# Kernel optimization log

Measured on AMD Instinct MI355X. Metric: run time of the kernel, lower is better.

## Reference

```python
import jax, jax.numpy as jnp
import numpy as np

B, S, D, H, DFF = 2, 4096, 256, 8, 1024
DK = D // H


def setup_inputs() -> dict:
    key = jax.random.key(0)
    ks = jax.random.split(key, 12)
    sc = 0.02
    inp = {
        "x": jax.random.normal(ks[0], (B, S, D), jnp.float32),
        "mask": jnp.ones((B, 1, 1, S), jnp.int32),
        "Wq": jax.random.normal(ks[1], (D, D), jnp.float32) * sc,
        "bq": jnp.zeros((D,), jnp.float32),
        "Wk": jax.random.normal(ks[2], (D, D), jnp.float32) * sc,
        "bk": jnp.zeros((D,), jnp.float32),
        "Wv": jax.random.normal(ks[3], (D, D), jnp.float32) * sc,
        "bv": jnp.zeros((D,), jnp.float32),
        "Wo": jax.random.normal(ks[4], (D, D), jnp.float32) * sc,
        "bo": jnp.zeros((D,), jnp.float32),
        "W1": jax.random.normal(ks[5], (D, DFF), jnp.float32) * sc,
        "b1": jnp.zeros((DFF,), jnp.float32),
        "W2": jax.random.normal(ks[6], (DFF, D), jnp.float32) * sc,
        "b2": jnp.zeros((D,), jnp.float32),
        "g1": jnp.ones((D,), jnp.float32),
        "be1": jnp.zeros((D,), jnp.float32),
        "g2": jnp.ones((D,), jnp.float32),
        "be2": jnp.zeros((D,), jnp.float32),
        "a1": jnp.float32(1e-8),
        "a2": jnp.float32(1e-8),
    }
    return inp


def _layernorm(x, g, b, eps=1e-5):
    mu = jnp.mean(x, axis=-1, keepdims=True)
    var = jnp.var(x, axis=-1, keepdims=True)
    return (x - mu) * jax.lax.rsqrt(var + eps) * g + b


def _block(x, mask, Wq, bq, Wk, bk, Wv, bv, Wo, bo, W1, b1, W2, b2, g1, be1, g2, be2, a1, a2):
    # multi-head attention (dropout = identity in eval)
    def proj(W, b):
        return (x @ W + b).reshape(B, S, H, DK).transpose(0, 2, 1, 3)  # [B,H,S,DK]
    q, k, v = proj(Wq, bq), proj(Wk, bk), proj(Wv, bv)
    scores = jnp.einsum("bhsd,bhtd->bhst", q, k) / jnp.sqrt(jnp.float32(DK))
    scores = jnp.where(mask == 0, jnp.float32(-1e9), scores)
    p_attn = jax.nn.softmax(scores, axis=-1)
    ctx = jnp.einsum("bhst,bhtd->bhsd", p_attn, v)
    ctx = ctx.transpose(0, 2, 1, 3).reshape(B, S, D)
    attn_out = ctx @ Wo + bo
    x1 = _layernorm(x + a1 * attn_out, g1, be1)
    # FFN
    h = jax.nn.gelu(x1 @ W1 + b1, approximate=False)
    ffn_out = h @ W2 + b2
    return _layernorm(x1 + a2 * ffn_out, g2, be2)


def reference(x, mask, Wq, bq, Wk, bk, Wv, bv, Wo, bo, W1, b1, W2, b2, g1, be1, g2, be2, a1, a2):
    return _block(x, mask, Wq, bq, Wk, bk, Wv, bv, Wo, bo, W1, b1, W2, b2, g1, be1, g2, be2, a1, a2)
```

## Files before the change

### kernel.cpp

```cpp
#include <hip/hip_runtime.h>
#include <hip/hip_bf16.h>
#include <math.h>

#define B_ 2
#define S_ 4096
#define D_ 256
#define H_ 8
#define DFF_ 1024
#define DK_ 32

typedef __attribute__((ext_vector_type(8))) short short8;
typedef __attribute__((ext_vector_type(4))) float f32x4;
typedef __attribute__((ext_vector_type(16))) float f32x16;
typedef __attribute__((ext_vector_type(4))) int int4v;

__device__ __forceinline__ unsigned short f2bf(float f) {
  unsigned int u = __builtin_bit_cast(unsigned int, f);
  u += 0x7FFFu + ((u >> 16) & 1u);
  return (unsigned short)(u >> 16);
}

__device__ __forceinline__ float bf2f(unsigned short s) {
  unsigned int u = ((unsigned int)s) << 16;
  return __builtin_bit_cast(float, u);
}

__device__ __forceinline__ short8 u32x4_to_s8(unsigned int a, unsigned int b,
                                              unsigned int c, unsigned int d) {
  int4v v = {(int)a, (int)b, (int)c, (int)d};
  return __builtin_bit_cast(short8, v);
}

__device__ __forceinline__ float gelu_fast(float v) {
  float e = __builtin_amdgcn_exp2f(v * fmaf(0.10294609f, v * v, 2.3022077f));
  float th = 1.0f - 2.0f * __builtin_amdgcn_rcpf(e + 1.0f);
  return 0.5f * v * (1.0f + th);
}

__global__ __launch_bounds__(256) void k_prepw(
    const float* __restrict__ Wq, const float* __restrict__ Wk,
    const float* __restrict__ Wv, const float* __restrict__ Wo,
    const float* __restrict__ W1, const float* __restrict__ W2,
    const float* __restrict__ bq, const float* __restrict__ bk,
    const float* __restrict__ bv, const float* __restrict__ x,
    unsigned short* __restrict__ WqkvT, unsigned short* __restrict__ WoT,
    unsigned short* __restrict__ W1T, unsigned short* __restrict__ W2T,
    float* __restrict__ bqkv, unsigned short* __restrict__ xb) {
  const float k2 = 0.25500525551f;
  int bx = blockIdx.x, t = threadIdx.x;

  if (bx < 192) {
    __shared__ float tile[64][65];
    const float* src;
    unsigned short* dst;
    int Ksz, Nsz, ti, tj;
    float scale = 1.0f;
    if (bx < 48) {
      int which = bx >> 4, s = bx & 15;
      src = (which == 0) ? Wq : (which == 1) ? Wk : Wv;
      dst = WqkvT + which * 65536;
      Ksz = 256; Nsz = 256; ti = s >> 2; tj = s & 3;
      if (which == 0) scale = k2;
    } else if (bx < 64) {
      int s = bx - 48;
      src = Wo; dst = WoT; Ksz = 256; Nsz = 256; ti = s >> 2; tj = s & 3;
    } else if (bx < 128) {
      int s = bx - 64;
      src = W1; dst = W1T; Ksz = 256; Nsz = 1024; ti = s >> 4; tj = s & 15;
    } else {
      int s = bx - 128;
      src = W2; dst = W2T; Ksz = 1024; Nsz = 256; ti = s >> 2; tj = s & 3;
    }
    int row0 = ti * 64, col0 = tj * 64;
    int c = t & 63, rg = t >> 6;
#pragma unroll
    for (int i = 0; i < 16; i++) {
      int rr = rg * 16 + i;
      tile[rr][c] = src[(size_t)(row0 + rr) * Nsz + col0 + c] * scale;
    }
    __syncthreads();
    int k = t & 63;
#pragma unroll
    for (int i = 0; i < 16; i++) {
      int nn = rg * 16 + i;
      dst[(size_t)(col0 + nn) * Ksz + row0 + k] = f2bf(tile[k][nn]);
    }
  } else if (bx == 192) {
#pragma unroll
    for (int j = 0; j < 3; j++) {
      int i = j * 256 + t;
      if (i < 768)
        bqkv[i] = (i < 256) ? bq[i] * k2 : (i < 512) ? bk[i - 256] : bv[i - 512];
    }
  } else {
    int i = (bx - 193) * 2048 + t * 8;
    f32x4 f0 = *(const f32x4*)(x + i);
    f32x4 f1 = *(const f32x4*)(x + i + 4);
    short8 o;
#pragma unroll
    for (int e = 0; e < 4; e++) { o[e] = (short)f2bf(f0[e]); o[e + 4] = (short)f2bf(f1[e]); }
    *(short8*)(xb + i) = o;
  }
}

__global__ __launch_bounds__(256) void k_gemmqkv(const unsigned short* __restrict__ A,
                                                 const unsigned short* __restrict__ Bt,
                                                 const float* __restrict__ bias,
                                                 unsigned short* __restrict__ qb,
                                                 unsigned short* __restrict__ kpk,
                                                 unsigned short* __restrict__ vpk) {
  const int K = 256;
  __shared__ unsigned short Al[128][40];
  __shared__ unsigned short Bl[128][40];
  const int tid = threadIdx.x;
  const int wid = tid >> 6, lane = tid & 63;
  const int lhi = lane >> 4, llo = lane & 15;
  const int wr = wid >> 1, wc = wid & 1;
  const int rowbase = wr * 64, colbase = wc * 64;
  const int bm = blockIdx.x, bn = blockIdx.y;

  f32x4 zero = {0.f, 0.f, 0.f, 0.f};
  f32x4 acc[4][4];
#pragma unroll
  for (int m = 0; m < 4; m++)
#pragma unroll
    for (int n = 0; n < 4; n++) acc[m][n] = zero;

  const int r0 = tid >> 2, c8 = (tid & 3) * 8;
  const unsigned short* A16a = A + (size_t)(bm * 128 + r0) * K + c8;
  const unsigned short* A16b = A + (size_t)(bm * 128 + r0 + 64) * K + c8;
  const unsigned short* Brow0 = Bt + (size_t)(bn * 128 + r0) * K + c8;
  const unsigned short* Brow1 = Bt + (size_t)(bn * 128 + r0 + 64) * K + c8;

  for (int kb = 0; kb < K; kb += 32) {
    __syncthreads();
    *(short8*)&Al[r0][c8] = *(const short8*)(A16a + kb);
    *(short8*)&Al[r0 + 64][c8] = *(const short8*)(A16b + kb);
    *(short8*)&Bl[r0][c8] = *(const short8*)(Brow0 + kb);
    *(short8*)&Bl[r0 + 64][c8] = *(const short8*)(Brow1 + kb);
    __syncthreads();
    short8 af[4], bf[4];
#pragma unroll
    for (int m = 0; m < 4; m++) af[m] = *(const short8*)&Al[rowbase + m * 16 + llo][lhi * 8];
#pragma unroll
    for (int n = 0; n < 4; n++) bf[n] = *(const short8*)&Bl[colbase + n * 16 + llo][lhi * 8];
#pragma unroll
    for (int m = 0; m < 4; m++)
#pragma unroll
      for (int n = 0; n < 4; n++)
        acc[m][n] = __builtin_amdgcn_mfma_f32_16x16x32_bf16(af[m], bf[n], acc[m][n], 0, 0, 0);
  }

#pragma unroll
  for (int m = 0; m < 4; m++)
#pragma unroll
    for (int n = 0; n < 4; n++)
#pragma unroll
      for (int r = 0; r < 4; r++) {
        int row = bm * 128 + rowbase + m * 16 + lhi * 4 + r;
        int gcol = bn * 128 + colbase + n * 16 + llo;
        int which = gcol >> 8;
        int col0 = gcol & 255;
        float v = acc[m][n][r] + bias[gcol];
        unsigned short bv = f2bf(v);
        int t = row & (S_ - 1), b = row >> 12;
        int h = col0 >> 5;
        if (which == 0) {
          qb[(size_t)row * 256 + col0] = bv;
        } else if (which == 1) {
          int c5 = col0 & 31, jj = (c5 >> 4) & 1, hik = (c5 >> 3) & 1, e = c5 & 7;
          int tile = t >> 6, i = (t >> 5) & 1, l31k = t & 31;
          size_t addr = (((size_t)(b * 8 + h) * 64 + tile) * 4 + i * 2 + jj) * 512 +
                        (hik * 32 + l31k) * 8 + e;
          kpk[addr] = bv;
        } else {
          int d = col0 & 31;
          int x5 = t >> 6, j = (t >> 3) & 7, kk = t & 7;
          size_t addr = (((size_t)(b * 8 + h) * 64 + x5) * 4 + (j >> 1)) * 512 +
                        ((j & 1) * 32 + d) * 8 + kk;
          vpk[addr] = bv;
        }
      }
}

__global__ __launch_bounds__(256) void k_gemm1(const unsigned short* __restrict__ A,
                                               const unsigned short* __restrict__ Bt,
                                               const float* __restrict__ bias,
                                               unsigned short* __restrict__ Cout,
                                               int M, int N, int K) {
  __shared__ unsigned short Al[128][40];
  __shared__ unsigned short Bl[128][40];
  const int tid = threadIdx.x;
  const int wid = tid >> 6, lane = tid & 63;
  const int lhi = lane >> 4, llo = lane & 15;
  const int wr = wid >> 1, wc = wid & 1;
  const int rowbase = wr * 64, colbase = wc * 64;
  const int bm = blockIdx.x, bn = blockIdx.y;

  f32x4 zero = {0.f, 0.f, 0.f, 0.f};
  f32x4 acc[4][4];
#pragma unroll
  for (int m = 0; m < 4; m++)
#pragma unroll
    for (int n = 0; n < 4; n++) acc[m][n] = zero;

  const int r0 = tid >> 2, c8 = (tid & 3) * 8;
  const unsigned short* A16a = A + (size_t)(bm * 128 + r0) * K + c8;
  const unsigned short* A16b = A + (size_t)(bm * 128 + r0 + 64) * K + c8;
  const unsigned short* Brow0 = Bt + (size_t)(bn * 128 + r0) * K + c8;
  const unsigned short* Brow1 = Bt + (size_t)(bn * 128 + r0 + 64) * K + c8;

  for (int kb = 0; kb < K; kb += 32) {
    __syncthreads();
    *(short8*)&Al[r0][c8] = *(const short8*)(A16a + kb);
    *(short8*)&Al[r0 + 64][c8] = *(const short8*)(A16b + kb);
    *(short8*)&Bl[r0][c8] = *(const short8*)(Brow0 + kb);
    *(short8*)&Bl[r0 + 64][c8] = *(const short8*)(Brow1 + kb);
    __syncthreads();
    short8 af[4], bf[4];
#pragma unroll
    for (int m = 0; m < 4; m++) af[m] = *(const short8*)&Al[rowbase + m * 16 + llo][lhi * 8];
#pragma unroll
    for (int n = 0; n < 4; n++) bf[n] = *(const short8*)&Bl[colbase + n * 16 + llo][lhi * 8];
#pragma unroll
    for (int m = 0; m < 4; m++)
#pragma unroll
      for (int n = 0; n < 4; n++)
        acc[m][n] = __builtin_amdgcn_mfma_f32_16x16x32_bf16(af[m], bf[n], acc[m][n], 0, 0, 0);
  }

#pragma unroll
  for (int m = 0; m < 4; m++)
#pragma unroll
    for (int n = 0; n < 4; n++)
#pragma unroll
      for (int r = 0; r < 4; r++) {
        int row = bm * 128 + rowbase + m * 16 + lhi * 4 + r;
        int col = bn * 128 + colbase + n * 16 + llo;
        float v = acc[m][n][r] + bias[col];
        Cout[(size_t)row * N + col] = f2bf(gelu_fast(v));
      }
}

template <int BASE16, int OUT32>
__global__ __launch_bounds__(512) void k_gemmln(const unsigned short* __restrict__ A,
                                                const unsigned short* __restrict__ Bt,
                                                const float* __restrict__ bias,
                                                const void* __restrict__ base,
                                                const float* __restrict__ alpha,
                                                const float* __restrict__ g,
                                                const float* __restrict__ be,
                                                void* __restrict__ y, int K) {
  __shared__ unsigned short Al[2][32][40];
  __shared__ unsigned short Bl[2][256][40];
  __shared__ float psum[32][4], psq[32][4];
  float* partial = (float*)&Bl[0][0][0];

  const int tid = threadIdx.x;
  const int w = tid >> 6, lane = tid & 63;
  const int kh = w >> 2, wc = w & 3;
  const int lhi = lane >> 4, llo = lane & 15;
  const int row0 = blockIdx.x * 32;
  const int Kh = K >> 1;

  f32x4 zero = {0.f, 0.f, 0.f, 0.f};
  f32x4 acc[2][4];
#pragma unroll
  for (int m = 0; m < 2; m++)
#pragma unroll
    for (int n = 0; n < 4; n++) acc[m][n] = zero;

  for (int kb = 0; kb < Kh; kb += 32) {
    __syncthreads();
    if (tid < 256) {
      int kh2 = tid >> 7, ra = (tid >> 2) & 31, ca = (tid & 3) * 8;
      *(short8*)&Al[kh2][ra][ca] =
          *(const short8*)(A + (size_t)(row0 + ra) * K + kh2 * Kh + kb + ca);
    }
#pragma unroll
    for (int s = 0; s < 4; s++) {
      int c = tid + s * 512;
      int kh2 = c >> 10, rb = (c >> 2) & 255, cb = (c & 3) * 8;
      *(short8*)&Bl[kh2][rb][cb] =
          *(const short8*)(Bt + (size_t)rb * K + kh2 * Kh + kb + cb);
    }
    __syncthreads();
    short8 af[2], bf[4];
#pragma unroll
    for (int m = 0; m < 2; m++) af[m] = *(const short8*)&Al[kh][m * 16 + llo][lhi * 8];
#pragma unroll
    for (int n = 0; n < 4; n++)
      bf[n] = *(const short8*)&Bl[kh][wc * 64 + n * 16 + llo][lhi * 8];
#pragma unroll
    for (int m = 0; m < 2; m++)
#pragma unroll
      for (int n = 0; n < 4; n++)
        acc[m][n] = __builtin_amdgcn_mfma_f32_16x16x32_bf16(af[m], bf[n], acc[m][n], 0, 0, 0);
  }

  __syncthreads();
  if (kh == 1) {
#pragma unroll
    for (int m = 0; m < 2; m++)
#pragma unroll
      for (int n = 0; n < 4; n++)
#pragma unroll
        for (int r = 0; r < 4; r++) {
          int lrow = m * 16 + lhi * 4 + r;
          int col = wc * 64 + n * 16 + llo;
          partial[lrow * 256 + col] = acc[m][n][r];
        }
  }
  __syncthreads();

  const float a = alpha[0];
  const unsigned short* b16 = (const unsigned short*)base;
  const float* b32 = (const float*)base;

  if (kh == 0) {
#pragma unroll
    for (int m = 0; m < 2; m++)
#pragma unroll
      for (int r = 0; r < 4; r++) {
        int lrow = m * 16 + lhi * 4 + r;
        size_t grow = (size_t)(row0 + lrow);
        float s = 0.f, q = 0.f;
#pragma unroll
        for (int n = 0; n < 4; n++) {
          int col = wc * 64 + n * 16 + llo;
          float v = acc[m][n][r] + partial[lrow * 256 + col] + bias[col];
          float xb = BASE16 ? bf2f(b16[grow * 256 + col]) : b32[grow * 256 + col];
          float rr = fmaf(a, v, xb);
          acc[m][n][r] = rr;
          s += rr;
          q = fmaf(rr, rr, q);
        }
#pragma unroll
        for (int off = 1; off < 16; off <<= 1) {
          s += __shfl_xor(s, off);
          q += __shfl_xor(q, off);
        }
        if (llo == 0) { psum[lrow][wc] = s; psq[lrow][wc] = q; }
      }
  }
  __syncthreads();

  if (kh == 0) {
#pragma unroll
    for (int m = 0; m < 2; m++)
#pragma unroll
      for (int r = 0; r < 4; r++) {
        int lrow = m * 16 + lhi * 4 + r;
        size_t grow = (size_t)(row0 + lrow);
        float S = psum[lrow][0] + psum[lrow][1] + psum[lrow][2] + psum[lrow][3];
        float Q = psq[lrow][0] + psq[lrow][1] + psq[lrow][2] + psq[lrow][3];
        float mu = S * (1.0f / 256.0f);
        float var = Q * (1.0f / 256.0f) - mu * mu;
        float rs = rsqrtf(var + 1e-5f);
#pragma unroll
        for (int n = 0; n < 4; n++) {
          int col = wc * 64 + n * 16 + llo;
          float o = (acc[m][n][r] - mu) * rs * g[col] + be[col];
          if (OUT32) ((float*)y)[grow * 256 + col] = o;
          else ((unsigned short*)y)[grow * 256 + col] = f2bf(o);
        }
      }
  }
}

__global__ __launch_bounds__(512, 2) void k_attn(const unsigned short* __restrict__ qb,
                                                 const unsigned short* __restrict__ kpk,
                                                 const unsigned short* __restrict__ vpk,
                                                 const int* __restrict__ mask,
                                                 unsigned short* __restrict__ ctx) {
  __shared__ float accS[4][32][32];
  __shared__ float lS[4][32];
  const int tid = threadIdx.x;
  const int lane = tid & 63;
  const int w = tid >> 6;
  const int qt = w >> 1, half = w & 1;
  const int l31 = lane & 31, hi = lane >> 5;
  const int q0 = blockIdx.x * 128 + qt * 32;
  const int h = blockIdx.y, b = blockIdx.z;
  const size_t bS = (size_t)b * S_;

  const unsigned short* Qp = qb + (bS + q0 + l31) * 256 + h * DK_ + hi * 8;
  short8 qf0 = *(const short8*)Qp;
  short8 qf1 = *(const short8*)(Qp + 16);

  const size_t fragbase = ((size_t)(b * H_ + h) * 64 + half * 32) * 2048 + lane * 8;
  const unsigned short* kp = kpk + fragbase;
  const unsigned short* vp = vpk + fragbase;
  const int* mp = mask + bS + half * 2048 + lane;

  f32x16 acc, lacc;
#pragma unroll
  for (int r = 0; r < 16; r++) { acc[r] = 0.f; lacc[r] = 0.f; }
  const f32x16 zz = acc;
  short8 ones;
#pragma unroll
  for (int e = 0; e < 8; e++) ones[e] = (short)0x3F80;

  short8 kf0, kf1, kf2, kf3, vf0, vf1, vf2, vf3;
  unsigned int pk0[8], pk1[8];
  f32x16 s0, s1;

#define LDKF() { kf0 = *(const short8*)(kp); kf1 = *(const short8*)(kp + 512); \
                 kf2 = *(const short8*)(kp + 1024); kf3 = *(const short8*)(kp + 1536); kp += 2048; }
#define LDVF() { vf0 = *(const short8*)(vp); vf1 = *(const short8*)(vp + 512); \
                 vf2 = *(const short8*)(vp + 1024); vf3 = *(const short8*)(vp + 1536); vp += 2048; }
#define QKM() {                                                                  \
    s0 = __builtin_amdgcn_mfma_f32_32x32x16_bf16(kf0, qf0, zz, 0, 0, 0);         \
    s1 = __builtin_amdgcn_mfma_f32_32x32x16_bf16(kf2, qf0, zz, 0, 0, 0);         \
    s0 = __builtin_amdgcn_mfma_f32_32x32x16_bf16(kf1, qf1, s0, 0, 0, 0);         \
    s1 = __builtin_amdgcn_mfma_f32_32x32x16_bf16(kf3, qf1, s1, 0, 0, 0);         \
  }
#define EXPM(mv) {                                                               \
    unsigned long long bal = __ballot((mv) != 0);                                \
    if (__builtin_expect(bal != ~0ull, 0)) {                                     \
      _Pragma("unroll") for (int r = 0; r < 16; r++) {                           \
        int tt = (r & 3) + 8 * (r >> 2) + 4 * hi;                                \
        if (!((bal >> tt) & 1)) s0[r] = -3e38f;                                  \
        if (!((bal >> (tt + 32)) & 1)) s1[r] = -3e38f;                           \
      }                                                                          \
    }                                                                            \
    _Pragma("unroll") for (int r = 0; r < 16; r++) {                             \
      s0[r] = __builtin_amdgcn_exp2f(s0[r]);                                     \
      s1[r] = __builtin_amdgcn_exp2f(s1[r]);                                     \
    }                                                                            \
    _Pragma("unroll") for (int j = 0; j < 8; j++) {                              \
      asm("v_cvt_pk_bf16_f32 %0, %1, %2" : "=v"(pk0[j]) : "v"(s0[2*j]), "v"(s0[2*j+1])); \
      asm("v_cvt_pk_bf16_f32 %0, %1, %2" : "=v"(pk1[j]) : "v"(s1[2*j]), "v"(s1[2*j+1])); \
    }                                                                            \
  }
#define PVM() {                                                                  \
    __builtin_amdgcn_s_setprio(1);                                               \
    _Pragma("unroll") for (int kk = 0; kk < 4; kk++) {                           \
      unsigned int* pk = (kk < 2) ? pk0 : pk1;                                   \
      int base = (kk & 1) * 4;                                                   \
      auto r02 = __builtin_amdgcn_permlane32_swap(pk[base], pk[base + 2], false, false);     \
      auto r13 = __builtin_amdgcn_permlane32_swap(pk[base + 1], pk[base + 3], false, false); \
      short8 pfr = u32x4_to_s8(r02[0], r13[0], r02[1], r13[1]);                  \
      short8 vv = (kk == 0) ? vf0 : (kk == 1) ? vf1 : (kk == 2) ? vf2 : vf3;     \
      acc = __builtin_amdgcn_mfma_f32_32x32x16_bf16(pfr, vv, acc, 0, 0, 0);      \
      lacc = __builtin_amdgcn_mfma_f32_32x32x16_bf16(pfr, ones, lacc, 0, 0, 0);  \
    }                                                                            \
    __builtin_amdgcn_s_setprio(0);                                               \
  }

  LDKF();
  int mvC = mp[0];
  int mvN = mp[64];
  QKM();
  LDKF();
  LDVF();
  EXPM(mvC);
  mvC = mvN;
  mvN = mp[128];

  for (int t = 1; t < 32; ++t) {
    QKM();
    LDKF();
    PVM();
    LDVF();
    EXPM(mvC);
    mvC = mvN;
    mvN = mp[(t + 2 < 32 ? t + 2 : 31) * 64];
  }
  PVM();

  if (half == 1) {
#pragma unroll
    for (int r = 0; r < 16; r++) {
      int q = (r & 3) + 8 * (r >> 2) + 4 * hi;
      accS[qt][q][l31] = acc[r];
    }
    if (l31 == 0) {
#pragma unroll
      for (int r = 0; r < 16; r++) {
        int q = (r & 3) + 8 * (r >> 2) + 4 * hi;
        lS[qt][q] = lacc[r];
      }
    }
  }
  __syncthreads();
  if (half == 0) {
#pragma unroll
    for (int r = 0; r < 16; r++) {
      int q = (r & 3) + 8 * (r >> 2) + 4 * hi;
      float o = acc[r] + accS[qt][q][l31];
      float L = lacc[r] + lS[qt][q];
      ctx[(bS + q0 + q) * (size_t)D_ + h * DK_ + l31] = f2bf(o / L);
    }
  }
#undef LDKF
#undef LDVF
#undef QKM
#undef EXPM
#undef PVM
}

extern "C" void kernel_launch(void* const* d_in, const int* in_sizes, int n_in,
                              void* d_out, int out_size, void* d_ws, size_t ws_size,
                              hipStream_t stream) {
  const float* x   = (const float*)d_in[0];
  const int* mask  = (const int*)d_in[1];
  const float* Wq  = (const float*)d_in[2];
  const float* bq  = (const float*)d_in[3];
  const float* Wk  = (const float*)d_in[4];
  const float* bk  = (const float*)d_in[5];
  const float* Wv  = (const float*)d_in[6];
  const float* bv  = (const float*)d_in[7];
  const float* Wo  = (const float*)d_in[8];
  const float* bo  = (const float*)d_in[9];
  const float* W1  = (const float*)d_in[10];
  const float* b1  = (const float*)d_in[11];
  const float* W2  = (const float*)d_in[12];
  const float* b2  = (const float*)d_in[13];
  const float* g1  = (const float*)d_in[14];
  const float* be1 = (const float*)d_in[15];
  const float* g2  = (const float*)d_in[16];
  const float* be2 = (const float*)d_in[17];
  const float* a1  = (const float*)d_in[18];
  const float* a2  = (const float*)d_in[19];
  float* out = (float*)d_out;

  char* ws = (char*)d_ws;
  const size_t MB = 1024 * 1024;
  unsigned short* qb  = (unsigned short*)(ws + 0);
  unsigned short* kpk = (unsigned short*)(ws + 5 * MB);
  unsigned short* vpk = (unsigned short*)(ws + 10 * MB);
  unsigned short* ctx = (unsigned short*)(ws + 15 * MB);
  unsigned short* x1b = (unsigned short*)(ws + 19 * MB);
  unsigned short* hb  = (unsigned short*)(ws + 23 * MB);
  unsigned short* WqkvT = (unsigned short*)(ws + 40 * MB);
  unsigned short* WoT   = (unsigned short*)(ws + 40 * MB + 512 * 1024);
  unsigned short* W1T   = (unsigned short*)(ws + 41 * MB);
  unsigned short* W2T   = (unsigned short*)(ws + 41 * MB + 512 * 1024);
  float* bqkv           = (float*)(ws + 42 * MB);
  unsigned short* xb    = (unsigned short*)(ws + 43 * MB);

  const int NTOK = B_ * S_;

  k_prepw<<<dim3(1217), 256, 0, stream>>>(Wq, Wk, Wv, Wo, W1, W2, bq, bk, bv, x,
                                          WqkvT, WoT, W1T, W2T, bqkv, xb);

  k_gemmqkv<<<dim3(64, 6), 256, 0, stream>>>(xb, WqkvT, bqkv, qb, kpk, vpk);

  k_attn<<<dim3(S_ / 128, H_, B_), 512, 0, stream>>>(qb, kpk, vpk, mask, ctx);

  k_gemmln<0, 0><<<dim3(NTOK / 32), 512, 0, stream>>>(ctx, WoT, bo, x, a1, g1, be1,
                                                      x1b, 256);

  k_gemm1<<<dim3(64, 8), 256, 0, stream>>>(x1b, W1T, b1, hb, NTOK, 1024, 256);

  k_gemmln<1, 1><<<dim3(NTOK / 32), 512, 0, stream>>>(hb, W2T, b2, x1b, a2, g2, be2,
                                                      out, 1024);
}
```

Measured before the change: 128.6 us.

## Reuse each K/V tile across two query blocks per wave in attention

The attention kernel changes from 512-thread blocks, where pairs of waves split the key range for 32 queries each, to 256-thread blocks of 64 queries. Each of the four waves now covers a quarter of the keys and applies every loaded K/V fragment to two 32-query sub-blocks. K and V are double-buffered in register arrays. This halves global K/V fragment loads per query and gives more MFMA work per load. The partial results of the four waves are reduced through a larger shared-memory buffer, at the cost of more registers and a longer final reduction.

```diff
diff --git a/kernel.cpp b/kernel.cpp
--- a/kernel.cpp
+++ b/kernel.cpp
@@ -368,60 +368,63 @@
   }
 }
 
-__global__ __launch_bounds__(512, 2) void k_attn(const unsigned short* __restrict__ qb,
+__global__ __launch_bounds__(256, 2) void k_attn(const unsigned short* __restrict__ qbuf,
                                                  const unsigned short* __restrict__ kpk,
                                                  const unsigned short* __restrict__ vpk,
                                                  const int* __restrict__ mask,
                                                  unsigned short* __restrict__ ctx) {
-  __shared__ float accS[4][32][32];
-  __shared__ float lS[4][32];
+  __shared__ float accS[4][64][32];
+  __shared__ float lS[4][64];
   const int tid = threadIdx.x;
   const int lane = tid & 63;
   const int w = tid >> 6;
-  const int qt = w >> 1, half = w & 1;
   const int l31 = lane & 31, hi = lane >> 5;
-  const int q0 = blockIdx.x * 128 + qt * 32;
+  const int q0 = blockIdx.x * 64;
   const int h = blockIdx.y, b = blockIdx.z;
   const size_t bS = (size_t)b * S_;
 
-  const unsigned short* Qp = qb + (bS + q0 + l31) * 256 + h * DK_ + hi * 8;
-  short8 qf0 = *(const short8*)Qp;
-  short8 qf1 = *(const short8*)(Qp + 16);
-
-  const size_t fragbase = ((size_t)(b * H_ + h) * 64 + half * 32) * 2048 + lane * 8;
+  const unsigned short* QpA = qbuf + (bS + q0 + l31) * 256 + h * DK_ + hi * 8;
+  short8 qa0 = *(const short8*)QpA;
+  short8 qa1 = *(const short8*)(QpA + 16);
+  const unsigned short* QpB = QpA + 32 * 256;
+  short8 qb0 = *(const short8*)QpB;
+  short8 qb1 = *(const short8*)(QpB + 16);
+
+  const size_t fragbase = ((size_t)(b * H_ + h) * 64 + w * 16) * 2048 + lane * 8;
   const unsigned short* kp = kpk + fragbase;
   const unsigned short* vp = vpk + fragbase;
-  const int* mp = mask + bS + half * 2048 + lane;
-
-  f32x16 acc, lacc;
-#pragma unroll
-  for (int r = 0; r < 16; r++) { acc[r] = 0.f; lacc[r] = 0.f; }
-  const f32x16 zz = acc;
+  const int* mp = mask + bS + w * 1024 + lane;
+
+  f32x16 accA, accB, laccA, laccB;
+#pragma unroll
+  for (int r = 0; r < 16; r++) { accA[r] = 0.f; accB[r] = 0.f; laccA[r] = 0.f; laccB[r] = 0.f; }
+  const f32x16 zz = accA;
   short8 ones;
 #pragma unroll
   for (int e = 0; e < 8; e++) ones[e] = (short)0x3F80;
 
-  short8 kf0, kf1, kf2, kf3, vf0, vf1, vf2, vf3;
+  short8 kA[4], vA[4], kB[4], vB[4];
   unsigned int pk0[8], pk1[8];
   f32x16 s0, s1;
-
-#define LDKF() { kf0 = *(const short8*)(kp); kf1 = *(const short8*)(kp + 512); \
-                 kf2 = *(const short8*)(kp + 1024); kf3 = *(const short8*)(kp + 1536); kp += 2048; }
-#define LDVF() { vf0 = *(const short8*)(vp); vf1 = *(const short8*)(vp + 512); \
-                 vf2 = *(const short8*)(vp + 1024); vf3 = *(const short8*)(vp + 1536); vp += 2048; }
-#define QKM() {                                                                  \
-    s0 = __builtin_amdgcn_mfma_f32_32x32x16_bf16(kf0, qf0, zz, 0, 0, 0);         \
-    s1 = __builtin_amdgcn_mfma_f32_32x32x16_bf16(kf2, qf0, zz, 0, 0, 0);         \
-    s0 = __builtin_amdgcn_mfma_f32_32x32x16_bf16(kf1, qf1, s0, 0, 0, 0);         \
-    s1 = __builtin_amdgcn_mfma_f32_32x32x16_bf16(kf3, qf1, s1, 0, 0, 0);         \
-  }
-#define EXPM(mv) {                                                               \
-    unsigned long long bal = __ballot((mv) != 0);                                \
-    if (__builtin_expect(bal != ~0ull, 0)) {                                     \
+  int tcur = 0;
+  int mvC, mvN;
+
+#define LDK(DST) { DST[0] = *(const short8*)(kp); DST[1] = *(const short8*)(kp + 512); \
+                   DST[2] = *(const short8*)(kp + 1024); DST[3] = *(const short8*)(kp + 1536); kp += 2048; }
+#define LDV(DST) { DST[0] = *(const short8*)(vp); DST[1] = *(const short8*)(vp + 512); \
+                   DST[2] = *(const short8*)(vp + 1024); DST[3] = *(const short8*)(vp + 1536); vp += 2048; }
+#define QKM(KF, qx0, qx1) {                                                      \
+    s0 = __builtin_amdgcn_mfma_f32_32x32x16_bf16(KF[0], qx0, zz, 0, 0, 0);       \
+    s1 = __builtin_amdgcn_mfma_f32_32x32x16_bf16(KF[2], qx0, zz, 0, 0, 0);       \
+    s0 = __builtin_amdgcn_mfma_f32_32x32x16_bf16(KF[1], qx1, s0, 0, 0, 0);       \
+    s1 = __builtin_amdgcn_mfma_f32_32x32x16_bf16(KF[3], qx1, s1, 0, 0, 0);       \
+  }
+#define EXPM(bal) {                                                              \
+    if (__builtin_expect((bal) != ~0ull, 0)) {                                   \
       _Pragma("unroll") for (int r = 0; r < 16; r++) {                           \
         int tt = (r & 3) + 8 * (r >> 2) + 4 * hi;                                \
-        if (!((bal >> tt) & 1)) s0[r] = -3e38f;                                  \
-        if (!((bal >> (tt + 32)) & 1)) s1[r] = -3e38f;                           \
+        if (!(((bal) >> tt) & 1)) s0[r] = -3e38f;                                \
+        if (!(((bal) >> (tt + 32)) & 1)) s1[r] = -3e38f;                         \
       }                                                                          \
     }                                                                            \
     _Pragma("unroll") for (int r = 0; r < 16; r++) {                             \
@@ -433,7 +436,7 @@
       asm("v_cvt_pk_bf16_f32 %0, %1, %2" : "=v"(pk1[j]) : "v"(s1[2*j]), "v"(s1[2*j+1])); \
     }                                                                            \
   }
-#define PVM() {                                                                  \
+#define PVM(VF, accX, laccX) {                                                   \
     __builtin_amdgcn_s_setprio(1);                                               \
     _Pragma("unroll") for (int kk = 0; kk < 4; kk++) {                           \
       unsigned int* pk = (kk < 2) ? pk0 : pk1;                                   \
@@ -441,63 +444,65 @@
       auto r02 = __builtin_amdgcn_permlane32_swap(pk[base], pk[base + 2], false, false);     \
       auto r13 = __builtin_amdgcn_permlane32_swap(pk[base + 1], pk[base + 3], false, false); \
       short8 pfr = u32x4_to_s8(r02[0], r13[0], r02[1], r13[1]);                  \
-      short8 vv = (kk == 0) ? vf0 : (kk == 1) ? vf1 : (kk == 2) ? vf2 : vf3;     \
-      acc = __builtin_amdgcn_mfma_f32_32x32x16_bf16(pfr, vv, acc, 0, 0, 0);      \
-      lacc = __builtin_amdgcn_mfma_f32_32x32x16_bf16(pfr, ones, lacc, 0, 0, 0);  \
+      accX = __builtin_amdgcn_mfma_f32_32x32x16_bf16(pfr, VF[kk], accX, 0, 0, 0);\
+      laccX = __builtin_amdgcn_mfma_f32_32x32x16_bf16(pfr, ones, laccX, 0, 0, 0);\
     }                                                                            \
     __builtin_amdgcn_s_setprio(0);                                               \
   }
-
-  LDKF();
-  int mvC = mp[0];
-  int mvN = mp[64];
-  QKM();
-  LDKF();
-  LDVF();
-  EXPM(mvC);
-  mvC = mvN;
-  mvN = mp[128];
-
-  for (int t = 1; t < 32; ++t) {
-    QKM();
-    LDKF();
-    PVM();
-    LDVF();
-    EXPM(mvC);
-    mvC = mvN;
-    mvN = mp[(t + 2 < 32 ? t + 2 : 31) * 64];
-  }
-  PVM();
-
-  if (half == 1) {
+#define TILESTEP(KC, VC, KN, VN) {                                               \
+    unsigned long long bal = __ballot(mvC != 0);                                 \
+    QKM(KC, qa0, qa1);                                                           \
+    LDK(KN);                                                                     \
+    EXPM(bal);                                                                   \
+    PVM(VC, accA, laccA);                                                        \
+    QKM(KC, qb0, qb1);                                                           \
+    LDV(VN);                                                                     \
+    EXPM(bal);                                                                   \
+    PVM(VC, accB, laccB);                                                        \
+    mvC = mvN;                                                                   \
+    tcur++;                                                                      \
+    mvN = mp[(tcur + 1 < 16 ? tcur + 1 : 15) * 64];                              \
+  }
+
+  LDK(kA);
+  LDV(vA);
+  mvC = mp[0];
+  mvN = mp[64];
+
+  for (int it = 0; it < 8; ++it) {
+    TILESTEP(kA, vA, kB, vB);
+    TILESTEP(kB, vB, kA, vA);
+  }
+
+#pragma unroll
+  for (int r = 0; r < 16; r++) {
+    int q = (r & 3) + 8 * (r >> 2) + 4 * hi;
+    accS[w][q][l31] = accA[r];
+    accS[w][q + 32][l31] = accB[r];
+  }
+  if (l31 == 0) {
 #pragma unroll
     for (int r = 0; r < 16; r++) {
       int q = (r & 3) + 8 * (r >> 2) + 4 * hi;
-      accS[qt][q][l31] = acc[r];
-    }
-    if (l31 == 0) {
-#pragma unroll
-      for (int r = 0; r < 16; r++) {
-        int q = (r & 3) + 8 * (r >> 2) + 4 * hi;
-        lS[qt][q] = lacc[r];
-      }
+      lS[w][q] = laccA[r];
+      lS[w][q + 32] = laccB[r];
     }
   }
   __syncthreads();
-  if (half == 0) {
-#pragma unroll
-    for (int r = 0; r < 16; r++) {
-      int q = (r & 3) + 8 * (r >> 2) + 4 * hi;
-      float o = acc[r] + accS[qt][q][l31];
-      float L = lacc[r] + lS[qt][q];
-      ctx[(bS + q0 + q) * (size_t)D_ + h * DK_ + l31] = f2bf(o / L);
-    }
-  }
-#undef LDKF
-#undef LDVF
+#pragma unroll
+  for (int i = 0; i < 8; i++) {
+    int e = tid + 256 * i;
+    int q = e >> 5, d = e & 31;
+    float o = accS[0][q][d] + accS[1][q][d] + accS[2][q][d] + accS[3][q][d];
+    float L = lS[0][q] + lS[1][q] + lS[2][q] + lS[3][q];
+    ctx[(bS + q0 + q) * (size_t)D_ + h * DK_ + d] = f2bf(o / L);
+  }
+#undef LDK
+#undef LDV
 #undef QKM
 #undef EXPM
 #undef PVM
+#undef TILESTEP
 }
 
 extern "C" void kernel_launch(void* const* d_in, const int* in_sizes, int n_in,
@@ -547,7 +552,7 @@
 
   k_gemmqkv<<<dim3(64, 6), 256, 0, stream>>>(xb, WqkvT, bqkv, qb, kpk, vpk);
 
-  k_attn<<<dim3(S_ / 128, H_, B_), 512, 0, stream>>>(qb, kpk, vpk, mask, ctx);
+  k_attn<<<dim3(S_ / 64, H_, B_), 256, 0, stream>>>(qb, kpk, vpk, mask, ctx);
 
   k_gemmln<0, 0><<<dim3(NTOK / 32), 512, 0, stream>>>(ctx, WoT, bo, x, a1, g1, be1,
                                                       x1b, 256);
```

Result: faster. 123.3 us (-4.1%).
